# Optimization experiments

Measured on AMD Instinct MI355X. Metric: run time of the kernel, lower is better.

Reference implementation:

```python
import jax, jax.numpy as jnp
import numpy as np

B, S, F, H = 2, 1024, 1024, 16  # H = n_heads arg; effective chunks Hc = F // H = 64, head_dim = H = 16


def _lin(x, w, b):
    # torch nn.Linear: y = x @ W^T + b, W has shape (out, in)
    return jnp.einsum('bsf,of->bso', x, w) + b


def setup_inputs() -> dict:
    key = jax.random.key(0)
    ks = jax.random.split(key, 16)
    sc = 0.02
    d = {'x': jax.random.normal(ks[0], (B, S, F), jnp.float32)}
    names = ['wq', 'wk', 'wv', 'vq', 'vk', 'vv', 'wo']
    for i, n in enumerate(names):
        d[n + '_w'] = jax.random.normal(ks[1 + 2 * i], (F, F), jnp.float32) * sc
        d[n + '_b'] = jax.random.normal(ks[2 + 2 * i], (F,), jnp.float32) * sc
    return d


def reference(x, wq_w, wq_b, wk_w, wk_b, wv_w, wv_b,
              vq_w, vq_b, vk_w, vk_b, vv_w, vv_b, wo_w, wo_b):
    b, s, f = x.shape
    hc = f // H  # number of chunks produced by torch.split(., n_heads, dim=-1)
    q = _lin(_lin(x, wq_w, wq_b), vq_w, vq_b)
    k = _lin(_lin(x, wk_w, wk_b), vk_w, vk_b)
    v = _lin(_lin(x, wv_w, wv_b), vv_w, vv_b)
    # split into hc chunks of size H along feature dim, concat on batch dim -> (hc, b, s, H)
    q = q.reshape(b, s, hc, H).transpose(2, 0, 1, 3)
    k = k.reshape(b, s, hc, H).transpose(2, 0, 1, 3)
    v = v.reshape(b, s, hc, H).transpose(2, 0, 1, 3)
    scale = jnp.sqrt(jnp.asarray(H, q.dtype))
    scores = jnp.einsum('cbqh,cbkh->cbqk', q, k) / scale  # (hc, b, s, s)
    attn = jax.nn.softmax(scores, axis=-1)
    o = jnp.einsum('cbqk,cbkh->cbqh', attn, v)  # (hc, b, s, H)
    # torch: view(H, b, s, f//H) then unsqueeze(-2).swapaxes(0,-2).reshape(b,s,f)
    o = o.reshape(H, b, s, hc).transpose(1, 2, 0, 3).reshape(b, s, f)
    return _lin(o, wo_w, wo_b)
```

## Files before the change

kernel.cpp:

```cpp
#include <hip/hip_runtime.h>
#include <hip/hip_bf16.h>
#include <stdint.h>

typedef __bf16 bf16_t;
typedef __bf16 bf16x8 __attribute__((ext_vector_type(8)));
typedef __bf16 bf16x4 __attribute__((ext_vector_type(4)));
typedef float f32x4 __attribute__((ext_vector_type(4)));
typedef float f32x16 __attribute__((ext_vector_type(16)));
typedef uint32_t u32x4 __attribute__((ext_vector_type(4)));

#define XN 2097152
#define WN 1048576

typedef __attribute__((address_space(1))) const uint8_t* gas_ptr;
typedef __attribute__((address_space(3))) uint8_t* las_ptr;

static __device__ __forceinline__ uint16_t bfbits(float f) {
    bf16_t b = (bf16_t)f;
    return __builtin_bit_cast(uint16_t, b);
}

__global__ void cast_k(const float* __restrict__ x,
    const float* __restrict__ a0, const float* __restrict__ a1,
    const float* __restrict__ a2, const float* __restrict__ a3,
    bf16_t* __restrict__ dst)
{
    const int TOTC = (XN + 4 * WN) / 4;
    for (int c = blockIdx.x * blockDim.x + threadIdx.x; c < TOTC; c += gridDim.x * blockDim.x) {
        int el = c * 4;
        const float* s;
        if (el < XN) {
            s = x + el;
        } else {
            int r = el - XN;
            int wi = r >> 20;
            int off = r & (WN - 1);
            const float* wp = (wi == 0) ? a0 : (wi == 1) ? a1 : (wi == 2) ? a2 : a3;
            s = wp + off;
        }
        float4 f = *(const float4*)s;
        bf16x4 o = { (bf16_t)f.x, (bf16_t)f.y, (bf16_t)f.z, (bf16_t)f.w };
        *(bf16x4*)(dst + el) = o;
    }
}

__global__ __launch_bounds__(256)
void trans_k(const float* __restrict__ s0, const float* __restrict__ s1,
             const float* __restrict__ s2, bf16_t* __restrict__ dstBase)
{
    const int gid = blockIdx.x;
    const int w = gid >> 6, t6 = gid & 63;
    const int r0 = (t6 >> 3) * 128, c0 = (t6 & 7) * 128;
    const float* src = (w == 0) ? s0 : (w == 1) ? s1 : s2;
    bf16_t* dst = dstBase + (size_t)w * WN;

    __shared__ uint8_t tt[32768];
    const int t = threadIdx.x;

#pragma unroll
    for (int i = 0; i < 4; ++i) {
        const int lid = i * 256 + t;
        const int r4 = lid >> 5, c4 = lid & 31;
        const float* p = src + (size_t)(r0 + r4 * 4) * 1024 + c0 + c4 * 4;
        float4 a = *(const float4*)p;
        float4 b = *(const float4*)(p + 1024);
        float4 cv = *(const float4*)(p + 2048);
        float4 d = *(const float4*)(p + 3072);
        const float* af = (const float*)&a; const float* bf = (const float*)&b;
        const float* cf = (const float*)&cv; const float* df = (const float*)&d;
#pragma unroll
        for (int j = 0; j < 4; ++j) {
            const int cc = c4 * 4 + j;
            const int g = r4 >> 1, h = r4 & 1;
            bf16x4 o = { (bf16_t)af[j], (bf16_t)bf[j], (bf16_t)cf[j], (bf16_t)df[j] };
            *(bf16x4*)(tt + cc * 256 + ((g ^ (cc & 15)) << 4) + h * 8) = o;
        }
    }
    __syncthreads();
#pragma unroll
    for (int j = 0; j < 8; ++j) {
        const int lid = j * 256 + t;
        const int cc = lid >> 4, g = lid & 15;
        bf16x8 v = *(const bf16x8*)(tt + cc * 256 + ((g ^ (cc & 15)) << 4));
        *(bf16x8*)(dst + (size_t)(c0 + cc) * 1024 + r0 + g * 8) = v;
    }
}

__global__ __launch_bounds__(256)
void biasc_k(const bf16_t* __restrict__ vbase,
             const float* __restrict__ bi0, const float* __restrict__ bi1, const float* __restrict__ bi2,
             const float* __restrict__ bo0, const float* __restrict__ bo1, const float* __restrict__ bo2,
             float* __restrict__ out)
{
    const int bid = blockIdx.x;
    const int z = bid >> 8;
    const int wave = threadIdx.x >> 6, lane = threadIdx.x & 63;
    const int o = (bid & 255) * 4 + wave;
    const float* bi = (z == 0) ? bi0 : (z == 1) ? bi1 : bi2;
    const float* bo = (z == 0) ? bo0 : (z == 1) ? bo1 : bo2;
    const bf16_t* row = vbase + (size_t)z * WN + (size_t)o * 1024;

    float sum = 0.f;
#pragma unroll
    for (int i = 0; i < 2; ++i) {
        const int j = (lane + 64 * i) * 8;
        bf16x8 v = *(const bf16x8*)(row + j);
        float4 f0 = *(const float4*)(bi + j);
        float4 f1 = *(const float4*)(bi + j + 4);
        sum += (float)v[0] * f0.x + (float)v[1] * f0.y + (float)v[2] * f0.z + (float)v[3] * f0.w;
        sum += (float)v[4] * f1.x + (float)v[5] * f1.y + (float)v[6] * f1.z + (float)v[7] * f1.w;
    }
#pragma unroll
    for (int off = 1; off < 64; off <<= 1) sum += __shfl_xor(sum, off, 64);
    if (lane == 0) out[z * 1024 + o] = sum + bo[o];
}

#define QSCALE 0.36067376022224085f

template<int EPI, int BN, bool HASBIAS, int MT, int NT, int NZ>
__global__ __launch_bounds__(256)
void gemm_k(const bf16_t* __restrict__ A0, const bf16_t* __restrict__ A1, const bf16_t* __restrict__ A2,
            const bf16_t* __restrict__ W0, const bf16_t* __restrict__ W1, const bf16_t* __restrict__ W2,
            const float* __restrict__ bias0, const float* __restrict__ bias1, const float* __restrict__ bias2,
            void* O0, void* O1, void* O2)
{
    constexpr int NACC = BN / 32;
    constexpr int TOT = MT * NT * NZ;
    const int bid = blockIdx.x;
    const int swz = (bid & 7) * (TOT / 8) + (bid >> 3);
    const int z = (NZ == 1) ? 0 : swz / (MT * NT);
    const int rr = swz % (MT * NT);
    const int mt = rr / NT, nt = rr % NT;

    const bf16_t* A = (z == 0) ? A0 : (z == 1) ? A1 : A2;
    const bf16_t* W = (z == 0) ? W0 : (z == 1) ? W1 : W2;
    const float* bias = (z == 0) ? bias0 : (z == 1) ? bias1 : bias2;
    void* Ov = (z == 0) ? O0 : (z == 1) ? O1 : O2;

    __shared__ bf16_t As[128 * 64];
    __shared__ bf16_t Bs[BN * 64];

    const int tid = threadIdx.x;
    const int lane = tid & 63, wave = tid >> 6;
    const int lo = lane & 15, hi = lane >> 4;
    const int wr = wave >> 1, wc = wave & 1;
    const int m0 = mt * 128, n0 = nt * BN;

    f32x4 acc[4][NACC] = {};

    for (int kt = 0; kt < 16; ++kt) {
        const int K0 = kt * 64;
        __syncthreads();
#pragma unroll
        for (int i = 0; i < 4; ++i) {
            const int cbase = i * 256 + wave * 64;
            const int c = cbase + lane;
            const int row = c >> 3, ko = c & 7;
            const bf16_t* ga = A + (size_t)(m0 + row) * 1024 + K0 + ko * 8;
            __builtin_amdgcn_global_load_lds((gas_ptr)ga, (las_ptr)(As + cbase * 8), 16, 0, 0);
        }
#pragma unroll
        for (int i = 0; i < NACC; ++i) {
            const int cbase = i * 256 + wave * 64;
            const int c = cbase + lane;
            const int row = c >> 3, ko = c & 7;
            const bf16_t* gb = W + (size_t)(n0 + row) * 1024 + K0 + ko * 8;
            __builtin_amdgcn_global_load_lds((gas_ptr)gb, (las_ptr)(Bs + cbase * 8), 16, 0, 0);
        }
        __syncthreads();
#pragma unroll
        for (int kk = 0; kk < 2; ++kk) {
            const int kb = kk * 32 + hi * 8;
            bf16x8 af[4], bfr[NACC];
#pragma unroll
            for (int m = 0; m < 4; ++m) af[m] = *(const bf16x8*)&As[(wr * 64 + m * 16 + lo) * 64 + kb];
#pragma unroll
            for (int n = 0; n < NACC; ++n) bfr[n] = *(const bf16x8*)&Bs[(wc * (BN / 2) + n * 16 + lo) * 64 + kb];
#pragma unroll
            for (int m = 0; m < 4; ++m)
#pragma unroll
                for (int n = 0; n < NACC; ++n)
                    acc[m][n] = __builtin_amdgcn_mfma_f32_16x16x32_bf16(af[m], bfr[n], acc[m][n], 0, 0, 0);
        }
    }

#pragma unroll
    for (int n = 0; n < NACC; ++n) {
        const int col = n0 + wc * (BN / 2) + n * 16 + lo;
        const float bv = HASBIAS ? bias[col] : 0.f;
#pragma unroll
        for (int m = 0; m < 4; ++m) {
            const int r0 = m0 + wr * 64 + m * 16 + hi * 4;
            if (EPI == 2) {
                float* O = (float*)Ov;
#pragma unroll
                for (int r = 0; r < 4; ++r)
                    O[(size_t)(r0 + r) * 1024 + col] = acc[m][n][r] + bv;
            } else if (EPI == 0 || z == 0) {
                bf16_t* O = (bf16_t*)Ov;
                const float sc = (EPI == 1) ? QSCALE : 1.0f;
#pragma unroll
                for (int r = 0; r < 4; ++r)
                    O[(size_t)(r0 + r) * 1024 + col] = (bf16_t)((acc[m][n][r] + bv) * sc);
            } else if (z == 1) {
                bf16_t* O = (bf16_t*)Ov;
                const int cch = col >> 4, h = col & 15;
                const int bb = r0 >> 10;
                const size_t sb = (size_t)(cch * 2 + bb) * 16384;
#pragma unroll
                for (int r = 0; r < 4; ++r) {
                    const int ss = (r0 + r) & 1023;
                    const int C = ((ss >> 5) << 6) + ((h >> 3) << 5) + (ss & 31);
                    O[sb + C * 8 + (h & 7)] = (bf16_t)(acc[m][n][r] + bv);
                }
            } else {
                bf16_t* O = (bf16_t*)Ov;
                const int cch = col >> 4, h = col & 15;
                const int bb = r0 >> 10;
                const int s0 = r0 & 1023;
                const int C = ((s0 >> 5) << 6) + (((s0 >> 4) & 1) << 5) + (((s0 >> 3) & 1) << 4) + h;
                bf16x4 pv = { (bf16_t)(acc[m][n][0] + bv), (bf16_t)(acc[m][n][1] + bv),
                              (bf16_t)(acc[m][n][2] + bv), (bf16_t)(acc[m][n][3] + bv) };
                *(bf16x4*)(O + (size_t)(cch * 2 + bb) * 16384 + C * 8 + (s0 & 7)) = pv;
            }
        }
    }
}

__global__ __launch_bounds__(512)
void attn_k(const bf16_t* __restrict__ qg, const bf16_t* __restrict__ kfr,
            const bf16_t* __restrict__ vfr, bf16_t* __restrict__ y)
{
    __shared__ bf16_t lds[32768];

    const int c = blockIdx.y, b = blockIdx.z;
    const int tid = threadIdx.x;
    const int lane = tid & 63, wave = tid >> 6;
    const int l31 = lane & 31, hi = lane >> 5;
    const int s = blockIdx.x * 256 + wave * 32 + l31;

    const bf16_t* kb = kfr + (size_t)(c * 2 + b) * 16384;
    const bf16_t* vb = vfr + (size_t)(c * 2 + b) * 16384;
#pragma unroll
    for (int i = 0; i < 4; ++i) {
        const int cbase = i * 512 + wave * 64;
        __builtin_amdgcn_global_load_lds((gas_ptr)(kb + (cbase + lane) * 8),
                                         (las_ptr)((uint8_t*)lds + cbase * 16), 16, 0, 0);
        __builtin_amdgcn_global_load_lds((gas_ptr)(vb + (cbase + lane) * 8),
                                         (las_ptr)((uint8_t*)lds + 32768 + cbase * 16), 16, 0, 0);
    }

    bf16x8 qf = *(const bf16x8*)(qg + ((size_t)(b * 1024 + s)) * 1024 + c * 16 + hi * 8);

    __syncthreads();

    f32x16 oacc = {};
    const f32x16 z16 = {};
    float den = 0.f;
    const int vslot = ((lane >> 5) * 16 + (lane & 15)) * 8;

    for (int jt = 0; jt < 32; ++jt) {
        bf16x8 kf  = *(const bf16x8*)&lds[jt * 512 + lane * 8];
        bf16x8 vf0 = *(const bf16x8*)&lds[16384 + jt * 512 + vslot];
        bf16x8 vf1 = *(const bf16x8*)&lds[16384 + jt * 512 + 256 + vslot];

        f32x16 st = __builtin_amdgcn_mfma_f32_32x32x16_bf16(kf, qf, z16, 0, 0, 0);

        float p[16];
#pragma unroll
        for (int r = 0; r < 16; ++r) { p[r] = __builtin_amdgcn_exp2f(st[r]); den += p[r]; }

        uint32_t pk[8];
#pragma unroll
        for (int w = 0; w < 8; ++w)
            pk[w] = (uint32_t)bfbits(p[2 * w]) | ((uint32_t)bfbits(p[2 * w + 1]) << 16);

        asm("v_permlane32_swap_b32 %0, %1" : "+v"(pk[0]), "+v"(pk[2]));
        asm("v_permlane32_swap_b32 %0, %1" : "+v"(pk[1]), "+v"(pk[3]));
        asm("v_permlane32_swap_b32 %0, %1" : "+v"(pk[4]), "+v"(pk[6]));
        asm("v_permlane32_swap_b32 %0, %1" : "+v"(pk[5]), "+v"(pk[7]));

        u32x4 f0v = { pk[0], pk[1], pk[2], pk[3] };
        u32x4 f1v = { pk[4], pk[5], pk[6], pk[7] };
        bf16x8 pf0 = __builtin_bit_cast(bf16x8, f0v);
        bf16x8 pf1 = __builtin_bit_cast(bf16x8, f1v);

        oacc = __builtin_amdgcn_mfma_f32_32x32x16_bf16(vf0, pf0, oacc, 0, 0, 0);
        oacc = __builtin_amdgcn_mfma_f32_32x32x16_bf16(vf1, pf1, oacc, 0, 0, 0);
    }

    float dtot = den + __shfl_xor(den, 32, 64);
    float rinv = 1.0f / dtot;

    const int bo = (c >> 1) & 1;
    const int so = (c & 1) * 512 + b * 256 + (s >> 2);
    const int f0i = (c >> 2) * 64 + (s & 3) * 16;
    bf16_t* yb = y + ((size_t)bo * 1024 + so) * 1024 + f0i + 4 * hi;
    bf16x4 o1 = { (bf16_t)(oacc[0] * rinv), (bf16_t)(oacc[1] * rinv),
                  (bf16_t)(oacc[2] * rinv), (bf16_t)(oacc[3] * rinv) };
    *(bf16x4*)(yb) = o1;
    bf16x4 o2 = { (bf16_t)(oacc[4] * rinv), (bf16_t)(oacc[5] * rinv),
                  (bf16_t)(oacc[6] * rinv), (bf16_t)(oacc[7] * rinv) };
    *(bf16x4*)(yb + 8) = o2;
}

extern "C" void kernel_launch(void* const* d_in, const int* in_sizes, int n_in,
                              void* d_out, int out_size, void* d_ws, size_t ws_size,
                              hipStream_t stream)
{
    (void)in_sizes; (void)n_in; (void)out_size; (void)ws_size;
    bf16_t* base = (bf16_t*)d_ws;
    bf16_t* xbf  = base;
    bf16_t* vbf  = base + XN;
    bf16_t* wobf = vbf + 3 * WN;
    bf16_t* wT   = wobf + WN;
    bf16_t* Wc   = wT + 3 * WN;
    float*  bqc  = (float*)(Wc + 3 * WN);
    bf16_t* q    = Wc + 3 * WN + 8192;
    bf16_t* kc   = q + XN;
    bf16_t* vc   = kc + XN;
    bf16_t* y    = vc + XN;

    cast_k<<<dim3(1024), dim3(256), 0, stream>>>(
        (const float*)d_in[0], (const float*)d_in[7], (const float*)d_in[9],
        (const float*)d_in[11], (const float*)d_in[13], base);

    trans_k<<<dim3(192), dim3(256), 0, stream>>>(
        (const float*)d_in[1], (const float*)d_in[3], (const float*)d_in[5], wT);

    biasc_k<<<dim3(768), dim3(256), 0, stream>>>(
        vbf, (const float*)d_in[2], (const float*)d_in[4], (const float*)d_in[6],
        (const float*)d_in[8], (const float*)d_in[10], (const float*)d_in[12], bqc);

    gemm_k<0, 64, false, 8, 16, 3><<<dim3(384), dim3(256), 0, stream>>>(
        vbf, vbf + WN, vbf + 2 * WN, wT, wT + WN, wT + 2 * WN,
        nullptr, nullptr, nullptr, Wc, Wc + WN, Wc + 2 * WN);

    gemm_k<1, 128, true, 16, 8, 3><<<dim3(384), dim3(256), 0, stream>>>(
        xbf, xbf, xbf, Wc, Wc + WN, Wc + 2 * WN,
        bqc, bqc + 1024, bqc + 2048, q, kc, vc);

    attn_k<<<dim3(4, 64, 2), dim3(512), 0, stream>>>(q, kc, vc, y);

    gemm_k<2, 64, true, 16, 16, 1><<<dim3(256), dim3(256), 0, stream>>>(
        y, y, y, wobf, wobf, wobf,
        (const float*)d_in[14], nullptr, nullptr, d_out, d_out, d_out);
}
```

Baseline: 204.4 us.

## Merge prep kernels into one launch and double-buffer GEMM LDS tiles

The three preprocessing kernels (cast, transpose, bias-combine) become a single kernel that dispatches on block index. The bias-combine now reads the fp32 weights directly, so it no longer depends on the cast output. The GEMM now double-buffers its A/B LDS tiles: the next k-tile's global-to-LDS load is issued before computing on the current tile, with one barrier per iteration instead of two. This doubles LDS use per block, which may lower occupancy, and removes two launch gaps.

```diff
diff --git a/kernel.cpp b/kernel.cpp
--- a/kernel.cpp
+++ b/kernel.cpp
@@ -20,99 +20,97 @@
     return __builtin_bit_cast(uint16_t, b);
 }
 
-__global__ void cast_k(const float* __restrict__ x,
-    const float* __restrict__ a0, const float* __restrict__ a1,
-    const float* __restrict__ a2, const float* __restrict__ a3,
-    bf16_t* __restrict__ dst)
+__global__ __launch_bounds__(256)
+void prep_k(const float* __restrict__ x,
+            const float* __restrict__ wq, const float* __restrict__ wk, const float* __restrict__ wv,
+            const float* __restrict__ vq, const float* __restrict__ vk, const float* __restrict__ vv,
+            const float* __restrict__ wo,
+            const float* __restrict__ bq1, const float* __restrict__ bk1, const float* __restrict__ bv1,
+            const float* __restrict__ bq2, const float* __restrict__ bk2, const float* __restrict__ bv2,
+            bf16_t* __restrict__ castDst,
+            bf16_t* __restrict__ wT,
+            float* __restrict__ bqc)
 {
-    const int TOTC = (XN + 4 * WN) / 4;
-    for (int c = blockIdx.x * blockDim.x + threadIdx.x; c < TOTC; c += gridDim.x * blockDim.x) {
-        int el = c * 4;
-        const float* s;
-        if (el < XN) {
-            s = x + el;
-        } else {
-            int r = el - XN;
-            int wi = r >> 20;
-            int off = r & (WN - 1);
-            const float* wp = (wi == 0) ? a0 : (wi == 1) ? a1 : (wi == 2) ? a2 : a3;
-            s = wp + off;
-        }
-        float4 f = *(const float4*)s;
-        bf16x4 o = { (bf16_t)f.x, (bf16_t)f.y, (bf16_t)f.z, (bf16_t)f.w };
-        *(bf16x4*)(dst + el) = o;
-    }
-}
-
-__global__ __launch_bounds__(256)
-void trans_k(const float* __restrict__ s0, const float* __restrict__ s1,
-             const float* __restrict__ s2, bf16_t* __restrict__ dstBase)
-{
-    const int gid = blockIdx.x;
-    const int w = gid >> 6, t6 = gid & 63;
-    const int r0 = (t6 >> 3) * 128, c0 = (t6 & 7) * 128;
-    const float* src = (w == 0) ? s0 : (w == 1) ? s1 : s2;
-    bf16_t* dst = dstBase + (size_t)w * WN;
-
     __shared__ uint8_t tt[32768];
+    const int bid = blockIdx.x;
     const int t = threadIdx.x;
 
-#pragma unroll
-    for (int i = 0; i < 4; ++i) {
-        const int lid = i * 256 + t;
-        const int r4 = lid >> 5, c4 = lid & 31;
-        const float* p = src + (size_t)(r0 + r4 * 4) * 1024 + c0 + c4 * 4;
-        float4 a = *(const float4*)p;
-        float4 b = *(const float4*)(p + 1024);
-        float4 cv = *(const float4*)(p + 2048);
-        float4 d = *(const float4*)(p + 3072);
-        const float* af = (const float*)&a; const float* bf = (const float*)&b;
-        const float* cf = (const float*)&cv; const float* df = (const float*)&d;
-#pragma unroll
-        for (int j = 0; j < 4; ++j) {
-            const int cc = c4 * 4 + j;
-            const int g = r4 >> 1, h = r4 & 1;
-            bf16x4 o = { (bf16_t)af[j], (bf16_t)bf[j], (bf16_t)cf[j], (bf16_t)df[j] };
-            *(bf16x4*)(tt + cc * 256 + ((g ^ (cc & 15)) << 4) + h * 8) = o;
-        }
-    }
-    __syncthreads();
-#pragma unroll
-    for (int j = 0; j < 8; ++j) {
-        const int lid = j * 256 + t;
-        const int cc = lid >> 4, g = lid & 15;
-        bf16x8 v = *(const bf16x8*)(tt + cc * 256 + ((g ^ (cc & 15)) << 4));
-        *(bf16x8*)(dst + (size_t)(c0 + cc) * 1024 + r0 + g * 8) = v;
-    }
-}
-
-__global__ __launch_bounds__(256)
-void biasc_k(const bf16_t* __restrict__ vbase,
-             const float* __restrict__ bi0, const float* __restrict__ bi1, const float* __restrict__ bi2,
-             const float* __restrict__ bo0, const float* __restrict__ bo1, const float* __restrict__ bo2,
-             float* __restrict__ out)
-{
-    const int bid = blockIdx.x;
-    const int z = bid >> 8;
-    const int wave = threadIdx.x >> 6, lane = threadIdx.x & 63;
-    const int o = (bid & 255) * 4 + wave;
-    const float* bi = (z == 0) ? bi0 : (z == 1) ? bi1 : bi2;
-    const float* bo = (z == 0) ? bo0 : (z == 1) ? bo1 : bo2;
-    const bf16_t* row = vbase + (size_t)z * WN + (size_t)o * 1024;
-
-    float sum = 0.f;
-#pragma unroll
-    for (int i = 0; i < 2; ++i) {
-        const int j = (lane + 64 * i) * 8;
-        bf16x8 v = *(const bf16x8*)(row + j);
-        float4 f0 = *(const float4*)(bi + j);
-        float4 f1 = *(const float4*)(bi + j + 4);
-        sum += (float)v[0] * f0.x + (float)v[1] * f0.y + (float)v[2] * f0.z + (float)v[3] * f0.w;
-        sum += (float)v[4] * f1.x + (float)v[5] * f1.y + (float)v[6] * f1.z + (float)v[7] * f1.w;
-    }
-#pragma unroll
-    for (int off = 1; off < 64; off <<= 1) sum += __shfl_xor(sum, off, 64);
-    if (lane == 0) out[z * 1024 + o] = sum + bo[o];
+    if (bid < 1024) {
+        const int TOTC = (XN + 4 * WN) / 4;
+        for (int c = bid * 256 + t; c < TOTC; c += 1024 * 256) {
+            int el = c * 4;
+            const float* s;
+            if (el < XN) {
+                s = x + el;
+            } else {
+                int r = el - XN;
+                int wi = r >> 20;
+                int off = r & (WN - 1);
+                const float* wp = (wi == 0) ? vq : (wi == 1) ? vk : (wi == 2) ? vv : wo;
+                s = wp + off;
+            }
+            float4 f = *(const float4*)s;
+            bf16x4 o = { (bf16_t)f.x, (bf16_t)f.y, (bf16_t)f.z, (bf16_t)f.w };
+            *(bf16x4*)(castDst + el) = o;
+        }
+    } else if (bid < 1216) {
+        const int gid = bid - 1024;
+        const int w = gid >> 6, t6 = gid & 63;
+        const int r0 = (t6 >> 3) * 128, c0 = (t6 & 7) * 128;
+        const float* src = (w == 0) ? wq : (w == 1) ? wk : wv;
+        bf16_t* dst = wT + (size_t)w * WN;
+
+#pragma unroll
+        for (int i = 0; i < 4; ++i) {
+            const int lid = i * 256 + t;
+            const int r4 = lid >> 5, c4 = lid & 31;
+            const float* p = src + (size_t)(r0 + r4 * 4) * 1024 + c0 + c4 * 4;
+            float4 a = *(const float4*)p;
+            float4 b = *(const float4*)(p + 1024);
+            float4 cv = *(const float4*)(p + 2048);
+            float4 d = *(const float4*)(p + 3072);
+            const float* af = (const float*)&a; const float* bf = (const float*)&b;
+            const float* cf = (const float*)&cv; const float* df = (const float*)&d;
+#pragma unroll
+            for (int j = 0; j < 4; ++j) {
+                const int cc = c4 * 4 + j;
+                const int g = r4 >> 1, h = r4 & 1;
+                bf16x4 o = { (bf16_t)af[j], (bf16_t)bf[j], (bf16_t)cf[j], (bf16_t)df[j] };
+                *(bf16x4*)(tt + cc * 256 + ((g ^ (cc & 15)) << 4) + h * 8) = o;
+            }
+        }
+        __syncthreads();
+#pragma unroll
+        for (int j = 0; j < 8; ++j) {
+            const int lid = j * 256 + t;
+            const int cc = lid >> 4, g = lid & 15;
+            bf16x8 v = *(const bf16x8*)(tt + cc * 256 + ((g ^ (cc & 15)) << 4));
+            *(bf16x8*)(dst + (size_t)(c0 + cc) * 1024 + r0 + g * 8) = v;
+        }
+    } else {
+        const int vbid = bid - 1216;
+        const int z = vbid >> 8;
+        const int wave = t >> 6, lane = t & 63;
+        const int o = (vbid & 255) * 4 + wave;
+        const float* bi = (z == 0) ? bq1 : (z == 1) ? bk1 : bv1;
+        const float* bo = (z == 0) ? bq2 : (z == 1) ? bk2 : bv2;
+        const float* row = ((z == 0) ? vq : (z == 1) ? vk : vv) + (size_t)o * 1024;
+
+        float sum = 0.f;
+#pragma unroll
+        for (int i = 0; i < 2; ++i) {
+            const int j = (lane + 64 * i) * 8;
+            float4 r0 = *(const float4*)(row + j);
+            float4 r1 = *(const float4*)(row + j + 4);
+            float4 f0 = *(const float4*)(bi + j);
+            float4 f1 = *(const float4*)(bi + j + 4);
+            sum += r0.x * f0.x + r0.y * f0.y + r0.z * f0.z + r0.w * f0.w;
+            sum += r1.x * f1.x + r1.y * f1.y + r1.z * f1.z + r1.w * f1.w;
+        }
+#pragma unroll
+        for (int off = 1; off < 64; off <<= 1) sum += __shfl_xor(sum, off, 64);
+        if (lane == 0) bqc[z * 1024 + o] = sum + bo[o];
+    }
 }
 
 #define QSCALE 0.36067376022224085f
@@ -137,8 +135,8 @@
     const float* bias = (z == 0) ? bias0 : (z == 1) ? bias1 : bias2;
     void* Ov = (z == 0) ? O0 : (z == 1) ? O1 : O2;
 
-    __shared__ bf16_t As[128 * 64];
-    __shared__ bf16_t Bs[BN * 64];
+    __shared__ bf16_t As[2][128 * 64];
+    __shared__ bf16_t Bs[2][BN * 64];
 
     const int tid = threadIdx.x;
     const int lane = tid & 63, wave = tid >> 6;
@@ -146,18 +144,15 @@
     const int wr = wave >> 1, wc = wave & 1;
     const int m0 = mt * 128, n0 = nt * BN;
 
-    f32x4 acc[4][NACC] = {};
-
-    for (int kt = 0; kt < 16; ++kt) {
+    auto stage = [&](int buf, int kt) {
         const int K0 = kt * 64;
-        __syncthreads();
 #pragma unroll
         for (int i = 0; i < 4; ++i) {
             const int cbase = i * 256 + wave * 64;
             const int c = cbase + lane;
             const int row = c >> 3, ko = c & 7;
             const bf16_t* ga = A + (size_t)(m0 + row) * 1024 + K0 + ko * 8;
-            __builtin_amdgcn_global_load_lds((gas_ptr)ga, (las_ptr)(As + cbase * 8), 16, 0, 0);
+            __builtin_amdgcn_global_load_lds((gas_ptr)ga, (las_ptr)(&As[buf][cbase * 8]), 16, 0, 0);
         }
 #pragma unroll
         for (int i = 0; i < NACC; ++i) {
@@ -165,23 +160,33 @@
             const int c = cbase + lane;
             const int row = c >> 3, ko = c & 7;
             const bf16_t* gb = W + (size_t)(n0 + row) * 1024 + K0 + ko * 8;
-            __builtin_amdgcn_global_load_lds((gas_ptr)gb, (las_ptr)(Bs + cbase * 8), 16, 0, 0);
-        }
-        __syncthreads();
+            __builtin_amdgcn_global_load_lds((gas_ptr)gb, (las_ptr)(&Bs[buf][cbase * 8]), 16, 0, 0);
+        }
+    };
+
+    f32x4 acc[4][NACC] = {};
+
+    stage(0, 0);
+    __syncthreads();
+
+    for (int kt = 0; kt < 16; ++kt) {
+        const int cur = kt & 1;
+        if (kt < 15) stage(cur ^ 1, kt + 1);
 #pragma unroll
         for (int kk = 0; kk < 2; ++kk) {
             const int kb = kk * 32 + hi * 8;
             bf16x8 af[4], bfr[NACC];
 #pragma unroll
-            for (int m = 0; m < 4; ++m) af[m] = *(const bf16x8*)&As[(wr * 64 + m * 16 + lo) * 64 + kb];
-#pragma unroll
-            for (int n = 0; n < NACC; ++n) bfr[n] = *(const bf16x8*)&Bs[(wc * (BN / 2) + n * 16 + lo) * 64 + kb];
+            for (int m = 0; m < 4; ++m) af[m] = *(const bf16x8*)&As[cur][(wr * 64 + m * 16 + lo) * 64 + kb];
+#pragma unroll
+            for (int n = 0; n < NACC; ++n) bfr[n] = *(const bf16x8*)&Bs[cur][(wc * (BN / 2) + n * 16 + lo) * 64 + kb];
 #pragma unroll
             for (int m = 0; m < 4; ++m)
 #pragma unroll
                 for (int n = 0; n < NACC; ++n)
                     acc[m][n] = __builtin_amdgcn_mfma_f32_16x16x32_bf16(af[m], bfr[n], acc[m][n], 0, 0, 0);
         }
+        __syncthreads();
     }
 
 #pragma unroll
@@ -321,16 +326,14 @@
     bf16_t* vc   = kc + XN;
     bf16_t* y    = vc + XN;
 
-    cast_k<<<dim3(1024), dim3(256), 0, stream>>>(
-        (const float*)d_in[0], (const float*)d_in[7], (const float*)d_in[9],
-        (const float*)d_in[11], (const float*)d_in[13], base);
-
-    trans_k<<<dim3(192), dim3(256), 0, stream>>>(
-        (const float*)d_in[1], (const float*)d_in[3], (const float*)d_in[5], wT);
-
-    biasc_k<<<dim3(768), dim3(256), 0, stream>>>(
-        vbf, (const float*)d_in[2], (const float*)d_in[4], (const float*)d_in[6],
-        (const float*)d_in[8], (const float*)d_in[10], (const float*)d_in[12], bqc);
+    prep_k<<<dim3(1984), dim3(256), 0, stream>>>(
+        (const float*)d_in[0],
+        (const float*)d_in[1], (const float*)d_in[3], (const float*)d_in[5],
+        (const float*)d_in[7], (const float*)d_in[9], (const float*)d_in[11],
+        (const float*)d_in[13],
+        (const float*)d_in[2], (const float*)d_in[4], (const float*)d_in[6],
+        (const float*)d_in[8], (const float*)d_in[10], (const float*)d_in[12],
+        base, wT, bqc);
 
     gemm_k<0, 64, false, 8, 16, 3><<<dim3(384), dim3(256), 0, stream>>>(
         vbf, vbf + WN, vbf + 2 * WN, wT, wT + WN, wT + 2 * WN,
```

Result: no change. 203.4 us (-0.5%).
